# Kernel tuning notes

Measured on AMD Instinct MI355X. Metric: run time of the kernel, lower is better.

The kernel has to match this reference:

```python
import jax, jax.numpy as jnp
import numpy as np

B, PRE, POST = 32, 2048, 2048
TAU_PRE = 2.0
TAU_POST = 2.0
V_TH = 1.0  # IF-neuron firing threshold


def setup_inputs() -> dict:
    key = jax.random.key(0)
    k1, k2, k3, k4 = jax.random.split(key, 4)
    # input spikes are binary (Bernoulli p=0.2)
    x = (jax.random.uniform(k1, (B, PRE)) < 0.2).astype(jnp.float32)
    # Linear weight [post, pre], Kaiming-ish scale
    W = jax.random.normal(k2, (POST, PRE), dtype=jnp.float32) / np.sqrt(PRE)
    # pre/post traces carried over from previous timesteps
    trace_pre = jax.random.uniform(k3, (B, PRE), dtype=jnp.float32)
    trace_post = jax.random.uniform(k4, (B, POST), dtype=jnp.float32)
    return {"x": x, "W": W, "trace_pre": trace_pre, "trace_post": trace_post}


def reference(x, W, trace_pre, trace_post):
    # connection: i = x @ W^T  -> [B, POST]
    i = x @ W.T
    # node: IF neuron, Heaviside spike
    spike = (i >= V_TH).astype(x.dtype)
    # trace decay (EMA) + spike accumulation
    tp = trace_pre - trace_pre / TAU_PRE + x        # [B, PRE]
    tq = trace_post - trace_post / TAU_POST + spike  # [B, POST]
    # clamp weight once; batch outer-product sums expressed as GEMMs
    Wc = jnp.clip(W, -1.0, 1.0)
    dw = (-Wc * jnp.einsum('bp,bq->pq', tq, x)
          + Wc * jnp.einsum('bp,bq->pq', spike, tp))  # [POST, PRE]
    return (spike, dw)
```

## Files before the change

kernel.cpp:

```cpp
#include <hip/hip_runtime.h>
#include <hip/hip_bf16.h>

#define B_ 32
#define PRE_ 2048
#define POST_ 2048

typedef __attribute__((ext_vector_type(8))) short short8;
typedef __attribute__((ext_vector_type(4))) float floatx4;

__device__ __forceinline__ unsigned short f2bf(float f) {
    unsigned u = __float_as_uint(f);
    u += 0x7FFF + ((u >> 16) & 1);
    return (unsigned short)(u >> 16);
}
__device__ __forceinline__ float bf2f(unsigned short h) {
    return __uint_as_float(((unsigned)h) << 16);
}


__global__ __launch_bounds__(256) void stdp_kernelA(
    const float* __restrict__ x, const float* __restrict__ W,
    const float* __restrict__ trace_pre, const float* __restrict__ trace_post,
    float* __restrict__ out, unsigned short* __restrict__ ws)
{
    unsigned short* spT  = ws;
    unsigned short* ntqh = ws + 65536;
    unsigned short* ntql = ws + 2 * 65536;
    unsigned short* tphT = ws + 3 * 65536;
    unsigned short* tplT = ws + 4 * 65536;
    unsigned short* xT   = ws + 5 * 65536;

    const int tid = threadIdx.x;
    const int bid = blockIdx.x;

    if (bid >= 128) {
        int lin  = (bid - 128) * 256 + tid;
        int base = lin * 4;
        int b = base >> 11, p = base & 2047;
        floatx4 xv = *(const floatx4*)(x + base);
        floatx4 tv = *(const floatx4*)(trace_pre + base);
#pragma unroll
        for (int j = 0; j < 4; ++j) {
            float tp = 0.5f * tv[j] + xv[j];
            unsigned short h = f2bf(tp);
            unsigned short l = f2bf(tp - bf2f(h));
            int o = (p + j) * B_ + b;
            tphT[o] = h; tplT[o] = l; xT[o] = f2bf(xv[j]);
        }
        return;
    }

    __shared__ unsigned short Wh[16][264];
    __shared__ unsigned short Wl[16][264];
    __shared__ float red[4 * 2 * 4 * 64];

    const int q0   = bid * 16;
    const int wave = tid >> 6, lane = tid & 63;
    const int quad = lane >> 4, l16 = lane & 15;

    floatx4 acc0 = {0.f, 0.f, 0.f, 0.f};
    floatx4 acc1 = {0.f, 0.f, 0.f, 0.f};

    for (int k0 = 0; k0 < PRE_; k0 += 256) {
#pragma unroll
        for (int i = 0; i < 4; ++i) {
            int id = tid + i * 256;
            int r = id >> 6, c = (id & 63) << 2;
            floatx4 wv = *(const floatx4*)(W + (q0 + r) * PRE_ + k0 + c);
#pragma unroll
            for (int j = 0; j < 4; ++j) {
                unsigned short h = f2bf(wv[j]);
                Wh[r][c + j] = h;
                Wl[r][c + j] = f2bf(wv[j] - bf2f(h));
            }
        }
        __syncthreads();
#pragma unroll
        for (int t = 0; t < 2; ++t) {
            int koff = (wave * 2 + t) * 32 + quad * 8;
            short8 bh = *(const short8*)&Wh[l16][koff];
            short8 bl = *(const short8*)&Wl[l16][koff];
            int kk = k0 + koff;
            const float* xp0 = x + l16 * PRE_ + kk;
            const float* xp1 = x + (16 + l16) * PRE_ + kk;
            floatx4 x0a = *(const floatx4*)xp0;
            floatx4 x0b = *(const floatx4*)(xp0 + 4);
            floatx4 x1a = *(const floatx4*)xp1;
            floatx4 x1b = *(const floatx4*)(xp1 + 4);
            short8 a0, a1;
#pragma unroll
            for (int j = 0; j < 4; ++j) {
                a0[j]     = (short)f2bf(x0a[j]);
                a0[j + 4] = (short)f2bf(x0b[j]);
                a1[j]     = (short)f2bf(x1a[j]);
                a1[j + 4] = (short)f2bf(x1b[j]);
            }
            acc0 = __builtin_amdgcn_mfma_f32_16x16x32_bf16(a0, bh, acc0, 0, 0, 0);
            acc0 = __builtin_amdgcn_mfma_f32_16x16x32_bf16(a0, bl, acc0, 0, 0, 0);
            acc1 = __builtin_amdgcn_mfma_f32_16x16x32_bf16(a1, bh, acc1, 0, 0, 0);
            acc1 = __builtin_amdgcn_mfma_f32_16x16x32_bf16(a1, bl, acc1, 0, 0, 0);
        }
        __syncthreads();
    }

#pragma unroll
    for (int r = 0; r < 4; ++r) {
        red[((wave * 2 + 0) * 4 + r) * 64 + lane] = acc0[r];
        red[((wave * 2 + 1) * 4 + r) * 64 + lane] = acc1[r];
    }
    __syncthreads();

    if (wave == 0) {
#pragma unroll
        for (int mt = 0; mt < 2; ++mt) {
#pragma unroll
            for (int r = 0; r < 4; ++r) {
                float s = 0.f;
#pragma unroll
                for (int w = 0; w < 4; ++w) s += red[((w * 2 + mt) * 4 + r) * 64 + lane];
                int b = mt * 16 + quad * 4 + r;
                int q = q0 + l16;
                float spike = (s >= 1.0f) ? 1.0f : 0.0f;
                out[b * POST_ + q] = spike;
                float tq = 0.5f * trace_post[b * POST_ + q] + spike;
                unsigned short h = f2bf(-tq);
                unsigned short l = f2bf(-tq - bf2f(h));
                int o = q * B_ + b;
                spT[o]  = f2bf(spike);
                ntqh[o] = h;
                ntql[o] = l;
            }
        }
    }
}

__global__ __launch_bounds__(256) void stdp_kernelB(
    const float* __restrict__ W, const unsigned short* __restrict__ ws,
    float* __restrict__ out)
{
    const unsigned short* spT  = ws;
    const unsigned short* ntqh = ws + 65536;
    const unsigned short* ntql = ws + 2 * 65536;
    const unsigned short* tphT = ws + 3 * 65536;
    const unsigned short* tplT = ws + 4 * 65536;
    const unsigned short* xT   = ws + 5 * 65536;
    float* dw = out + B_ * POST_;

    const int tid  = threadIdx.x;
    const int wave = tid >> 6, lane = tid & 63;
    const int quad = lane >> 4, l16 = lane & 15;
    const int qb = blockIdx.x >> 5, pb = blockIdx.x & 31;
    const int q0 = qb * 64, p0 = pb * 64;

    const int pw = p0 + wave * 16 + l16;
    short8 fx  = *(const short8*)(xT   + pw * B_ + quad * 8);
    short8 fth = *(const short8*)(tphT + pw * B_ + quad * 8);
    short8 ftl = *(const short8*)(tplT + pw * B_ + quad * 8);

#pragma unroll
    for (int qt = 0; qt < 4; ++qt) {
        int q = q0 + qt * 16 + l16;
        short8 fs  = *(const short8*)(spT  + q * B_ + quad * 8);
        short8 fnh = *(const short8*)(ntqh + q * B_ + quad * 8);
        short8 fnl = *(const short8*)(ntql + q * B_ + quad * 8);
        floatx4 acc = {0.f, 0.f, 0.f, 0.f};
        acc = __builtin_amdgcn_mfma_f32_16x16x32_bf16(fs,  fth, acc, 0, 0, 0);
        acc = __builtin_amdgcn_mfma_f32_16x16x32_bf16(fs,  ftl, acc, 0, 0, 0);
        acc = __builtin_amdgcn_mfma_f32_16x16x32_bf16(fnh, fx,  acc, 0, 0, 0);
        acc = __builtin_amdgcn_mfma_f32_16x16x32_bf16(fnl, fx,  acc, 0, 0, 0);
#pragma unroll
        for (int r = 0; r < 4; ++r) {
            int qq = q0 + qt * 16 + quad * 4 + r;
            float wv = W[qq * PRE_ + pw];
            wv = fminf(fmaxf(wv, -1.0f), 1.0f);
            dw[qq * PRE_ + pw] = wv * acc[r];
        }
    }
}

extern "C" void kernel_launch(void* const* d_in, const int* in_sizes, int n_in,
                              void* d_out, int out_size, void* d_ws, size_t ws_size,
                              hipStream_t stream) {
    const float* x     = (const float*)d_in[0];
    const float* W     = (const float*)d_in[1];
    const float* tpre  = (const float*)d_in[2];
    const float* tpost = (const float*)d_in[3];
    float* out = (float*)d_out;
    unsigned short* ws = (unsigned short*)d_ws;

    hipLaunchKernelGGL(stdp_kernelA, dim3(192), dim3(256), 0, stream,
                       x, W, tpre, tpost, out, ws);
    hipLaunchKernelGGL(stdp_kernelB, dim3(1024), dim3(256), 0, stream,
                       W, ws, out);
}
```

Baseline: 97.72 us.

## Fuse forward GEMM and dw outer-product into one kernel with LDS-resident W rows

Replaces the two-kernel split with a small prep kernel and one fused kernel. The prep kernel writes bf16 x (row-major and transposed) and the split trace_pre. The fused kernel loads 8 full W rows into LDS as hi/lo bf16 once, computes the spikes for those rows, keeps the spike and trace_post operands in LDS, and then produces the dw rows from the same LDS-resident W. This removes the second global read of W and the workspace round-trip for the post-side operands. In exchange it uses large LDS (about 66KB), so occupancy is low, half the MFMA output columns are discarded since QT=8 is below the 16-wide tile, and the grid is only 256 blocks.

Result: faster. 93.76 us (-4.0%).

```diff
diff --git a/kernel.cpp b/kernel.cpp
--- a/kernel.cpp
+++ b/kernel.cpp
@@ -1,11 +1,13 @@
 #include <hip/hip_runtime.h>
-#include <hip/hip_bf16.h>
 
 #define B_ 32
 #define PRE_ 2048
 #define POST_ 2048
+#define QT 8
+#define WPAD 2056
 
 typedef __attribute__((ext_vector_type(8))) short short8;
+typedef __attribute__((ext_vector_type(4))) short short4v;
 typedef __attribute__((ext_vector_type(4))) float floatx4;
 
 __device__ __forceinline__ unsigned short f2bf(float f) {
@@ -18,91 +20,77 @@
 }
 
 
-__global__ __launch_bounds__(256) void stdp_kernelA(
-    const float* __restrict__ x, const float* __restrict__ W,
-    const float* __restrict__ trace_pre, const float* __restrict__ trace_post,
-    float* __restrict__ out, unsigned short* __restrict__ ws)
+__global__ __launch_bounds__(256) void stdp_prep(
+    const float* __restrict__ x, const float* __restrict__ trace_pre,
+    unsigned short* __restrict__ ws)
 {
-    unsigned short* spT  = ws;
-    unsigned short* ntqh = ws + 65536;
-    unsigned short* ntql = ws + 2 * 65536;
-    unsigned short* tphT = ws + 3 * 65536;
-    unsigned short* tplT = ws + 4 * 65536;
-    unsigned short* xT   = ws + 5 * 65536;
+    int lin  = blockIdx.x * 256 + threadIdx.x;
+    int base = lin * 4;
+    int b = base >> 11, p = base & 2047;
+    floatx4 xv = *(const floatx4*)(x + base);
+    floatx4 tv = *(const floatx4*)(trace_pre + base);
+    short4v xr;
+#pragma unroll
+    for (int j = 0; j < 4; ++j) {
+        float tp = 0.5f * tv[j] + xv[j];
+        unsigned short h = f2bf(tp);
+        unsigned short l = f2bf(tp - bf2f(h));
+        int o = (p + j) * B_ + b;
+        ws[65536 + o]     = h;
+        ws[2 * 65536 + o] = l;
+        ws[3 * 65536 + o] = f2bf(xv[j]);
+        xr[j] = (short)f2bf(xv[j]);
+    }
+    *(short4v*)(ws + base) = xr;
+}
 
-    const int tid = threadIdx.x;
-    const int bid = blockIdx.x;
+__global__ __launch_bounds__(512) void stdp_fused(
+    const float* __restrict__ W, const float* __restrict__ trace_post,
+    const unsigned short* __restrict__ ws, float* __restrict__ out)
+{
+    __shared__ __align__(16) unsigned short Wh[QT * WPAD];
+    __shared__ __align__(16) unsigned short Wl[QT * WPAD];
+    __shared__ __align__(16) float red[8 * 2 * 4 * 64];
+    __shared__ __align__(16) unsigned short spA[QT * 32];
+    __shared__ __align__(16) unsigned short nqh[QT * 32];
+    __shared__ __align__(16) unsigned short nql[QT * 32];
 
-    if (bid >= 128) {
-        int lin  = (bid - 128) * 256 + tid;
-        int base = lin * 4;
-        int b = base >> 11, p = base & 2047;
-        floatx4 xv = *(const floatx4*)(x + base);
-        floatx4 tv = *(const floatx4*)(trace_pre + base);
+    const int tid  = threadIdx.x;
+    const int wave = tid >> 6, lane = tid & 63;
+    const int quad = lane >> 4, l16 = lane & 15;
+    const int q0   = blockIdx.x * QT;
+    const int qb   = l16 & 7;
+
+#pragma unroll
+    for (int it = 0; it < 8; ++it) {
+        int id = tid + it * 512;
+        int r  = id >> 9;
+        int c  = (id & 511) << 2;
+        floatx4 wv = *(const floatx4*)(W + (q0 + r) * PRE_ + c);
 #pragma unroll
         for (int j = 0; j < 4; ++j) {
-            float tp = 0.5f * tv[j] + xv[j];
-            unsigned short h = f2bf(tp);
-            unsigned short l = f2bf(tp - bf2f(h));
-            int o = (p + j) * B_ + b;
-            tphT[o] = h; tplT[o] = l; xT[o] = f2bf(xv[j]);
+            unsigned short h = f2bf(wv[j]);
+            Wh[r * WPAD + c + j] = h;
+            Wl[r * WPAD + c + j] = f2bf(wv[j] - bf2f(h));
         }
-        return;
     }
+    __syncthreads();
 
-    __shared__ unsigned short Wh[16][264];
-    __shared__ unsigned short Wl[16][264];
-    __shared__ float red[4 * 2 * 4 * 64];
-
-    const int q0   = bid * 16;
-    const int wave = tid >> 6, lane = tid & 63;
-    const int quad = lane >> 4, l16 = lane & 15;
-
+    const unsigned short* xrow = ws;
     floatx4 acc0 = {0.f, 0.f, 0.f, 0.f};
     floatx4 acc1 = {0.f, 0.f, 0.f, 0.f};
-
-    for (int k0 = 0; k0 < PRE_; k0 += 256) {
 #pragma unroll
-        for (int i = 0; i < 4; ++i) {
-            int id = tid + i * 256;
-            int r = id >> 6, c = (id & 63) << 2;
-            floatx4 wv = *(const floatx4*)(W + (q0 + r) * PRE_ + k0 + c);
-#pragma unroll
-            for (int j = 0; j < 4; ++j) {
-                unsigned short h = f2bf(wv[j]);
-                Wh[r][c + j] = h;
-                Wl[r][c + j] = f2bf(wv[j] - bf2f(h));
-            }
-        }
-        __syncthreads();
-#pragma unroll
-        for (int t = 0; t < 2; ++t) {
-            int koff = (wave * 2 + t) * 32 + quad * 8;
-            short8 bh = *(const short8*)&Wh[l16][koff];
-            short8 bl = *(const short8*)&Wl[l16][koff];
-            int kk = k0 + koff;
-            const float* xp0 = x + l16 * PRE_ + kk;
-            const float* xp1 = x + (16 + l16) * PRE_ + kk;
-            floatx4 x0a = *(const floatx4*)xp0;
-            floatx4 x0b = *(const floatx4*)(xp0 + 4);
-            floatx4 x1a = *(const floatx4*)xp1;
-            floatx4 x1b = *(const floatx4*)(xp1 + 4);
-            short8 a0, a1;
-#pragma unroll
-            for (int j = 0; j < 4; ++j) {
-                a0[j]     = (short)f2bf(x0a[j]);
-                a0[j + 4] = (short)f2bf(x0b[j]);
-                a1[j]     = (short)f2bf(x1a[j]);
-                a1[j + 4] = (short)f2bf(x1b[j]);
-            }
-            acc0 = __builtin_amdgcn_mfma_f32_16x16x32_bf16(a0, bh, acc0, 0, 0, 0);
-            acc0 = __builtin_amdgcn_mfma_f32_16x16x32_bf16(a0, bl, acc0, 0, 0, 0);
-            acc1 = __builtin_amdgcn_mfma_f32_16x16x32_bf16(a1, bh, acc1, 0, 0, 0);
-            acc1 = __builtin_amdgcn_mfma_f32_16x16x32_bf16(a1, bl, acc1, 0, 0, 0);
-        }
-        __syncthreads();
+    for (int s = 0; s < 8; ++s) {
+        int ko = wave * 256 + s * 32 + quad * 8;
+        short8 a0 = *(const short8*)(xrow + l16 * PRE_ + ko);
+        short8 a1 = *(const short8*)(xrow + (16 + l16) * PRE_ + ko);
+        short8 bh = *(const short8*)(Wh + qb * WPAD + ko);
+        short8 bl = *(const short8*)(Wl + qb * WPAD + ko);
+        acc0 = __builtin_amdgcn_mfma_f32_16x16x32_bf16(a0, bh, acc0, 0, 0, 0);
+        acc0 = __builtin_amdgcn_mfma_f32_16x16x32_bf16(a0, bl, acc0, 0, 0, 0);
+        acc1 = __builtin_amdgcn_mfma_f32_16x16x32_bf16(a1, bh, acc1, 0, 0, 0);
+        acc1 = __builtin_amdgcn_mfma_f32_16x16x32_bf16(a1, bl, acc1, 0, 0, 0);
     }
-
 #pragma unroll
     for (int r = 0; r < 4; ++r) {
         red[((wave * 2 + 0) * 4 + r) * 64 + lane] = acc0[r];
@@ -110,70 +98,56 @@
     }
     __syncthreads();
 
-    if (wave == 0) {
+    if (wave < 2 && l16 < QT) {
+        int mt = wave;
+        int q  = q0 + l16;
 #pragma unroll
-        for (int mt = 0; mt < 2; ++mt) {
+        for (int r = 0; r < 4; ++r) {
+            float s = 0.f;
 #pragma unroll
-            for (int r = 0; r < 4; ++r) {
-                float s = 0.f;
-#pragma unroll
-                for (int w = 0; w < 4; ++w) s += red[((w * 2 + mt) * 4 + r) * 64 + lane];
-                int b = mt * 16 + quad * 4 + r;
-                int q = q0 + l16;
-                float spike = (s >= 1.0f) ? 1.0f : 0.0f;
-                out[b * POST_ + q] = spike;
-                float tq = 0.5f * trace_post[b * POST_ + q] + spike;
-                unsigned short h = f2bf(-tq);
-                unsigned short l = f2bf(-tq - bf2f(h));
-                int o = q * B_ + b;
-                spT[o]  = f2bf(spike);
-                ntqh[o] = h;
-                ntql[o] = l;
-            }
+            for (int w = 0; w < 8; ++w) s += red[((w * 2 + mt) * 4 + r) * 64 + lane];
+            int b = mt * 16 + quad * 4 + r;
+            float spike = (s >= 1.0f) ? 1.0f : 0.0f;
+            out[b * POST_ + q] = spike;
+            float ntq = -(0.5f * trace_post[b * POST_ + q] + spike);
+            unsigned short h = f2bf(ntq);
+            unsigned short l = f2bf(ntq - bf2f(h));
+            spA[l16 * 32 + b] = f2bf(spike);
+            nqh[l16 * 32 + b] = h;
+            nql[l16 * 32 + b] = l;
         }
     }
-}
+    __syncthreads();
 
-__global__ __launch_bounds__(256) void stdp_kernelB(
-    const float* __restrict__ W, const unsigned short* __restrict__ ws,
-    float* __restrict__ out)
-{
-    const unsigned short* spT  = ws;
-    const unsigned short* ntqh = ws + 65536;
-    const unsigned short* ntql = ws + 2 * 65536;
-    const unsigned short* tphT = ws + 3 * 65536;
-    const unsigned short* tplT = ws + 4 * 65536;
-    const unsigned short* xT   = ws + 5 * 65536;
+    const unsigned short* tpTh = ws + 65536;
+    const unsigned short* tpTl = ws + 2 * 65536;
+    const unsigned short* xT   = ws + 3 * 65536;
     float* dw = out + B_ * POST_;
 
-    const int tid  = threadIdx.x;
-    const int wave = tid >> 6, lane = tid & 63;
-    const int quad = lane >> 4, l16 = lane & 15;
-    const int qb = blockIdx.x >> 5, pb = blockIdx.x & 31;
-    const int q0 = qb * 64, p0 = pb * 64;
+    short8 fs  = *(const short8*)(spA + qb * 32 + quad * 8);
+    short8 fnh = *(const short8*)(nqh + qb * 32 + quad * 8);
+    short8 fnl = *(const short8*)(nql + qb * 32 + quad * 8);
 
-    const int pw = p0 + wave * 16 + l16;
-    short8 fx  = *(const short8*)(xT   + pw * B_ + quad * 8);
-    short8 fth = *(const short8*)(tphT + pw * B_ + quad * 8);
-    short8 ftl = *(const short8*)(tplT + pw * B_ + quad * 8);
-
-#pragma unroll
-    for (int qt = 0; qt < 4; ++qt) {
-        int q = q0 + qt * 16 + l16;
-        short8 fs  = *(const short8*)(spT  + q * B_ + quad * 8);
-        short8 fnh = *(const short8*)(ntqh + q * B_ + quad * 8);
-        short8 fnl = *(const short8*)(ntql + q * B_ + quad * 8);
+#pragma unroll 2
+    for (int it = 0; it < 16; ++it) {
+        int p0 = (wave * 16 + it) * 16;
+        int p  = p0 + l16;
+        short8 fth = *(const short8*)(tpTh + p * 32 + quad * 8);
+        short8 ftl = *(const short8*)(tpTl + p * 32 + quad * 8);
+        short8 fx  = *(const short8*)(xT   + p * 32 + quad * 8);
         floatx4 acc = {0.f, 0.f, 0.f, 0.f};
         acc = __builtin_amdgcn_mfma_f32_16x16x32_bf16(fs,  fth, acc, 0, 0, 0);
         acc = __builtin_amdgcn_mfma_f32_16x16x32_bf16(fs,  ftl, acc, 0, 0, 0);
         acc = __builtin_amdgcn_mfma_f32_16x16x32_bf16(fnh, fx,  acc, 0, 0, 0);
         acc = __builtin_amdgcn_mfma_f32_16x16x32_bf16(fnl, fx,  acc, 0, 0, 0);
+        if (quad < 2) {
 #pragma unroll
-        for (int r = 0; r < 4; ++r) {
-            int qq = q0 + qt * 16 + quad * 4 + r;
-            float wv = W[qq * PRE_ + pw];
-            wv = fminf(fmaxf(wv, -1.0f), 1.0f);
-            dw[qq * PRE_ + pw] = wv * acc[r];
+            for (int r = 0; r < 4; ++r) {
+                int qd = quad * 4 + r;
+                float wv = bf2f(Wh[qd * WPAD + p]) + bf2f(Wl[qd * WPAD + p]);
+                wv = fminf(fmaxf(wv, -1.0f), 1.0f);
+                dw[(q0 + qd) * PRE_ + p] = wv * acc[r];
+            }
         }
     }
 }
@@ -188,8 +162,7 @@
     float* out = (float*)d_out;
     unsigned short* ws = (unsigned short*)d_ws;
 
-    hipLaunchKernelGGL(stdp_kernelA, dim3(192), dim3(256), 0, stream,
-                       x, W, tpre, tpost, out, ws);
-    hipLaunchKernelGGL(stdp_kernelB, dim3(1024), dim3(256), 0, stream,
-                       W, ws, out);
+    hipLaunchKernelGGL(stdp_prep, dim3(64), dim3(256), 0, stream, x, tpre, ws);
+    hipLaunchKernelGGL(stdp_fused, dim3(POST_ / QT / 1), dim3(512), 0, stream,
+                       W, tpost, ws, out);
 }
```
